# Kernel tuning notes

Hardware: AMD Instinct MI355X
Metric: run time of the kernel (lower is better)

Reference implementation:

```python
import jax, jax.numpy as jnp
import numpy as np

N, C = 65536, 100
TEMP = 2.0


def setup_inputs() -> dict:
    key = jax.random.key(0)
    ks = jax.random.split(key, 7)
    inp = {}
    names = ["outputs1", "outputs2", "outputs3", "outputs4", "outputs5", "mimic"]
    for k, name in zip(ks[:6], names):
        inp[name] = jax.random.normal(k, (N, C), dtype=jnp.float32)
    inp["targets"] = jax.random.randint(ks[6], (N,), 0, C, dtype=jnp.int64)
    inp["n_test"] = N
    return inp


def _margin(x, targets):
    # top-2 values per row; margin = top1-top2 if the target class is the argmax, else 0
    top2, _ = jax.lax.top_k(x, 2)  # [N, 2]
    tgt_val = jnp.take_along_axis(x, targets[:, None], axis=1)[:, 0]  # [N]
    return jnp.where(tgt_val == top2[:, 0], top2[:, 0] - top2[:, 1],
                     jnp.zeros((), dtype=x.dtype))


def reference(outputs1, outputs2, outputs3, outputs4, outputs5, mimic, targets, n_test):
    margins = jnp.stack(
        [_margin(o, targets) for o in (outputs1, outputs2, outputs3, outputs4, outputs5, mimic)],
        axis=-1,
    )  # [n_test, 6]
    out_threshold = jax.nn.softmax(margins / TEMP, axis=-1)
    max_preds = jnp.max(jnp.stack([outputs1, outputs2, outputs3, outputs4, outputs5], axis=0))
    return (max_preds, out_threshold)
```

## Files before the change

### kernel.cpp

```cpp
#include <hip/hip_runtime.h>


constexpr int C = 100;
constexpr int ROWS = 64;
constexpr int F4_PER_ROW = 25;
constexpr int F4_PER_TILE = ROWS * F4_PER_ROW;
constexpr float INV_TEMP = 0.5f;

typedef __attribute__((address_space(3))) void       as3_void;
typedef const __attribute__((address_space(1))) void as1_void;

__device__ __forceinline__ unsigned enc_f(float f) {
    unsigned u = __float_as_uint(f);
    return (u & 0x80000000u) ? ~u : (u | 0x80000000u);
}

__global__ __launch_bounds__(64) void margin_kernel(
    const float* __restrict__ o1, const float* __restrict__ o2,
    const float* __restrict__ o3, const float* __restrict__ o4,
    const float* __restrict__ o5, const float* __restrict__ mimic,
    const int* __restrict__ tgt, float* __restrict__ out,
    unsigned* __restrict__ ws, int n)
{
    __shared__ float4 tile[F4_PER_TILE];

    const int lane = threadIdx.x;
    const int m    = blockIdx.y;
    const int row0 = blockIdx.x * ROWS;

    const float* __restrict__ mat =
        (m == 0) ? o1 : (m == 1) ? o2 : (m == 2) ? o3 :
        (m == 3) ? o4 : (m == 4) ? o5 : mimic;

    const int pidx  = 2 * lane + 1;
    const int probe = (pidx < n) ? tgt[pidx] : 0;
    const unsigned long long nz = __ballot(probe != 0);
    const int tstride = (nz == 0ull) ? 2 : 1;

    const float4* __restrict__ src4 =
        (const float4*)mat + (size_t)row0 * F4_PER_ROW;
    const int f4_valid = (n - row0) * F4_PER_ROW;
    #pragma unroll
    for (int k = 0; k < F4_PER_ROW; ++k) {
        const int c = k * 64 + lane;
        if (c < f4_valid) {
            __builtin_amdgcn_global_load_lds((as1_void*)(src4 + c),
                                             (as3_void*)(tile + k * 64),
                                             16, 0, 0);
        }
    }
    __builtin_amdgcn_s_waitcnt(0);
    __syncthreads();

    float gmax = -INFINITY;
    const int row = row0 + lane;
    if (row < n) {
        const float4* __restrict__ p = tile + lane * F4_PER_ROW;
        float m1x = -INFINITY, m2x = -INFINITY;
        float m1y = -INFINITY, m2y = -INFINITY;
        float m1z = -INFINITY, m2z = -INFINITY;
        float m1w = -INFINITY, m2w = -INFINITY;
        #pragma unroll
        for (int i = 0; i < F4_PER_ROW; ++i) {
            const float4 v = p[i];
            m2x = fmaxf(m2x, fminf(m1x, v.x)); m1x = fmaxf(m1x, v.x);
            m2y = fmaxf(m2y, fminf(m1y, v.y)); m1y = fmaxf(m1y, v.y);
            m2z = fmaxf(m2z, fminf(m1z, v.z)); m1z = fmaxf(m1z, v.z);
            m2w = fmaxf(m2w, fminf(m1w, v.w)); m1w = fmaxf(m1w, v.w);
        }
        const float m1xy = fmaxf(m1x, m1y);
        const float m2xy = fmaxf(fminf(m1x, m1y), fmaxf(m2x, m2y));
        const float m1zw = fmaxf(m1z, m1w);
        const float m2zw = fmaxf(fminf(m1z, m1w), fmaxf(m2z, m2w));
        const float m1   = fmaxf(m1xy, m1zw);
        const float m2   = fmaxf(fminf(m1xy, m1zw), fmaxf(m2xy, m2zw));

        const int   t  = tgt[(size_t)row * tstride];
        const float tv = ((const float*)p)[t];
        out[1 + (size_t)row * 6 + m] = (tv == m1) ? (m1 - m2) * INV_TEMP : 0.0f;
        if (m < 5) gmax = m1;
    }

    if (m < 5) {
        #pragma unroll
        for (int s = 1; s < 64; s <<= 1) gmax = fmaxf(gmax, __shfl_xor(gmax, s));
        if (lane == 0) atomicMax(ws, enc_f(gmax));
    }
}

__global__ __launch_bounds__(256) void softmax_kernel(
    float* __restrict__ out, const unsigned* __restrict__ ws, int n)
{
    const int row = blockIdx.x * blockDim.x + threadIdx.x;
    if (row < n) {
        float* p = out + 1 + (size_t)row * 6;
        float mrg[6];
        #pragma unroll
        for (int j = 0; j < 6; ++j) mrg[j] = p[j];
        float mx = mrg[0];
        #pragma unroll
        for (int j = 1; j < 6; ++j) mx = fmaxf(mx, mrg[j]);
        float e[6], s = 0.0f;
        #pragma unroll
        for (int j = 0; j < 6; ++j) { e[j] = __expf(mrg[j] - mx); s += e[j]; }
        const float inv = 1.0f / s;
        #pragma unroll
        for (int j = 0; j < 6; ++j) p[j] = e[j] * inv;
    }
    if (row == 0) {
        const unsigned e = ws[0];
        const unsigned bits = (e & 0x80000000u) ? (e & 0x7FFFFFFFu) : ~e;
        out[0] = __uint_as_float(bits);
    }
}

extern "C" void kernel_launch(void* const* d_in, const int* in_sizes, int n_in,
                              void* d_out, int out_size, void* d_ws, size_t ws_size,
                              hipStream_t stream) {
    const float* o1    = (const float*)d_in[0];
    const float* o2    = (const float*)d_in[1];
    const float* o3    = (const float*)d_in[2];
    const float* o4    = (const float*)d_in[3];
    const float* o5    = (const float*)d_in[4];
    const float* mimic = (const float*)d_in[5];
    const int*   tgt   = (const int*)d_in[6];
    float*       out   = (float*)d_out;
    unsigned*    ws    = (unsigned*)d_ws;

    const int n = in_sizes[6];

    hipMemsetAsync(ws, 0, sizeof(unsigned), stream);

    dim3 grid((n + ROWS - 1) / ROWS, 6);
    margin_kernel<<<grid, 64, 0, stream>>>(o1, o2, o3, o4, o5, mimic,
                                           tgt, out, ws, n);
    softmax_kernel<<<(n + 255) / 256, 256, 0, stream>>>(out, ws, n);
}
```

Measured before the change: 209.0 us.

## Split each row across two threads with direct global loads instead of LDS staging

Drops the global_load_lds staging of 64-row tiles into shared memory. Each row is now processed by two adjacent threads that read float4s straight from global memory, and their top-2 results are merged with a lane shuffle. Blocks grow to 256 threads, and the per-block max is reduced through shared memory before one atomic per block. This removes the LDS round trip and the waitcnt barrier and raises parallelism, but each thread's global reads are strided by the 400-byte row pitch, so accesses are less coalesced.

```diff
diff --git a/kernel.cpp b/kernel.cpp
--- a/kernel.cpp
+++ b/kernel.cpp
@@ -2,31 +2,27 @@
 
 
 constexpr int C = 100;
-constexpr int ROWS = 64;
-constexpr int F4_PER_ROW = 25;
-constexpr int F4_PER_TILE = ROWS * F4_PER_ROW;
 constexpr float INV_TEMP = 0.5f;
-
-typedef __attribute__((address_space(3))) void       as3_void;
-typedef const __attribute__((address_space(1))) void as1_void;
 
 __device__ __forceinline__ unsigned enc_f(float f) {
     unsigned u = __float_as_uint(f);
     return (u & 0x80000000u) ? ~u : (u | 0x80000000u);
 }
 
-__global__ __launch_bounds__(64) void margin_kernel(
+__global__ __launch_bounds__(256) void margin_kernel(
     const float* __restrict__ o1, const float* __restrict__ o2,
     const float* __restrict__ o3, const float* __restrict__ o4,
     const float* __restrict__ o5, const float* __restrict__ mimic,
     const int* __restrict__ tgt, float* __restrict__ out,
     unsigned* __restrict__ ws, int n)
 {
-    __shared__ float4 tile[F4_PER_TILE];
+    __shared__ unsigned wmax[4];
 
-    const int lane = threadIdx.x;
     const int m    = blockIdx.y;
-    const int row0 = blockIdx.x * ROWS;
+    const int tid2 = blockIdx.x * 256 + threadIdx.x;
+    const int row  = tid2 >> 1;
+    const int half = tid2 & 1;
+    const int lane = threadIdx.x & 63;
 
     const float* __restrict__ mat =
         (m == 0) ? o1 : (m == 1) ? o2 : (m == 2) ? o3 :
@@ -37,32 +33,27 @@
     const unsigned long long nz = __ballot(probe != 0);
     const int tstride = (nz == 0ull) ? 2 : 1;
 
-    const float4* __restrict__ src4 =
-        (const float4*)mat + (size_t)row0 * F4_PER_ROW;
-    const int f4_valid = (n - row0) * F4_PER_ROW;
-    #pragma unroll
-    for (int k = 0; k < F4_PER_ROW; ++k) {
-        const int c = k * 64 + lane;
-        if (c < f4_valid) {
-            __builtin_amdgcn_global_load_lds((as1_void*)(src4 + c),
-                                             (as3_void*)(tile + k * 64),
-                                             16, 0, 0);
-        }
-    }
-    __builtin_amdgcn_s_waitcnt(0);
-    __syncthreads();
+    float rowM1 = -INFINITY;
 
-    float gmax = -INFINITY;
-    const int row = row0 + lane;
     if (row < n) {
-        const float4* __restrict__ p = tile + lane * F4_PER_ROW;
+        const size_t rowoff = (size_t)row * C;
+        const float4* __restrict__ p4 =
+            (const float4*)(mat + rowoff) + (half ? 13 : 0);
+
         float m1x = -INFINITY, m2x = -INFINITY;
         float m1y = -INFINITY, m2y = -INFINITY;
         float m1z = -INFINITY, m2z = -INFINITY;
         float m1w = -INFINITY, m2w = -INFINITY;
         #pragma unroll
-        for (int i = 0; i < F4_PER_ROW; ++i) {
-            const float4 v = p[i];
+        for (int i = 0; i < 12; ++i) {
+            const float4 v = p4[i];
+            m2x = fmaxf(m2x, fminf(m1x, v.x)); m1x = fmaxf(m1x, v.x);
+            m2y = fmaxf(m2y, fminf(m1y, v.y)); m1y = fmaxf(m1y, v.y);
+            m2z = fmaxf(m2z, fminf(m1z, v.z)); m1z = fmaxf(m1z, v.z);
+            m2w = fmaxf(m2w, fminf(m1w, v.w)); m1w = fmaxf(m1w, v.w);
+        }
+        if (!half) {
+            const float4 v = p4[12];
             m2x = fmaxf(m2x, fminf(m1x, v.x)); m1x = fmaxf(m1x, v.x);
             m2y = fmaxf(m2y, fminf(m1y, v.y)); m1y = fmaxf(m1y, v.y);
             m2z = fmaxf(m2z, fminf(m1z, v.z)); m1z = fmaxf(m1z, v.z);
@@ -72,19 +63,30 @@
         const float m2xy = fmaxf(fminf(m1x, m1y), fmaxf(m2x, m2y));
         const float m1zw = fmaxf(m1z, m1w);
         const float m2zw = fmaxf(fminf(m1z, m1w), fmaxf(m2z, m2w));
-        const float m1   = fmaxf(m1xy, m1zw);
-        const float m2   = fmaxf(fminf(m1xy, m1zw), fmaxf(m2xy, m2zw));
+        const float tm1  = fmaxf(m1xy, m1zw);
+        const float tm2  = fmaxf(fminf(m1xy, m1zw), fmaxf(m2xy, m2zw));
+
+        const float p1 = __shfl_xor(tm1, 1);
+        const float p2 = __shfl_xor(tm2, 1);
+        const float M1 = fmaxf(tm1, p1);
+        const float M2 = fmaxf(fminf(tm1, p1), fmaxf(tm2, p2));
 
         const int   t  = tgt[(size_t)row * tstride];
-        const float tv = ((const float*)p)[t];
-        out[1 + (size_t)row * 6 + m] = (tv == m1) ? (m1 - m2) * INV_TEMP : 0.0f;
-        if (m < 5) gmax = m1;
+        const float tv = mat[rowoff + t];
+        if (!half)
+            out[1 + (size_t)row * 6 + m] = (tv == M1) ? (M1 - M2) * INV_TEMP : 0.0f;
+        rowM1 = M1;
     }
 
+    #pragma unroll
+    for (int s = 1; s < 64; s <<= 1) rowM1 = fmaxf(rowM1, __shfl_xor(rowM1, s));
     if (m < 5) {
-        #pragma unroll
-        for (int s = 1; s < 64; s <<= 1) gmax = fmaxf(gmax, __shfl_xor(gmax, s));
-        if (lane == 0) atomicMax(ws, enc_f(gmax));
+        if (lane == 0) wmax[threadIdx.x >> 6] = enc_f(rowM1);
+        __syncthreads();
+        if (threadIdx.x == 0) {
+            const unsigned u = max(max(wmax[0], wmax[1]), max(wmax[2], wmax[3]));
+            atomicMax(ws, u);
+        }
     }
 }
 
@@ -131,8 +133,8 @@
 
     hipMemsetAsync(ws, 0, sizeof(unsigned), stream);
 
-    dim3 grid((n + ROWS - 1) / ROWS, 6);
-    margin_kernel<<<grid, 64, 0, stream>>>(o1, o2, o3, o4, o5, mimic,
-                                           tgt, out, ws, n);
+    dim3 grid((2 * n + 255) / 256, 6);
+    margin_kernel<<<grid, 256, 0, stream>>>(o1, o2, o3, o4, o5, mimic,
+                                            tgt, out, ws, n);
     softmax_kernel<<<(n + 255) / 256, 256, 0, stream>>>(out, ws, n);
 }
```

Result: faster. 186.6 us (-10.7%).
